# Optimization experiments

Measured on AMD Instinct MI355X. Metric: run time of the kernel, lower is better.

Reference implementation:

```python
import jax, jax.numpy as jnp
import numpy as np
from jax import lax

K = 3
STRIDE = 1
PAD = 1


def setup_inputs() -> dict:
    key = jax.random.key(0)
    k1, k2, k3, k4 = jax.random.split(key, 4)
    B, C, H, W = 4, 64, 128, 128
    O = 64
    x = jax.random.normal(k1, (B, C, H, W), dtype=jnp.float32)
    weight = jax.random.normal(k2, (O, C, K, K), dtype=jnp.float32) * 0.05
    bias = jax.random.normal(k3, (O,), dtype=jnp.float32) * 0.05
    # original zero-inits offset_conv (degenerate); use small random weights instead
    offset_w = jax.random.normal(k4, (2 * K * K, C, 3, 3), dtype=jnp.float32) * 0.01
    offset_b = jnp.zeros((2 * K * K,), dtype=jnp.float32)
    return {"x": x, "weight": weight, "bias": bias, "offset_w": offset_w, "offset_b": offset_b}


def _deform_conv(x, weight, bias, offset_w, offset_b):
    B, C, H, W = x.shape
    O = weight.shape[0]
    K2 = K * K
    # offset predictor: 3x3 conv, pad 1, stride 1 -> [B, 2*K2, H, W]
    offsets = lax.conv_general_dilated(
        x, offset_w, window_strides=(1, 1), padding=[(1, 1), (1, 1)],
        dimension_numbers=("NCHW", "OIHW", "NCHW")) + offset_b[None, :, None, None]

    Ho = (H - K + 2 * PAD) // STRIDE + 1
    Wo = (W - K + 2 * PAD) // STRIDE + 1
    padded = jnp.pad(x, ((0, 0), (0, 0), (PAD, PAD), (PAD, PAD)))
    Hp, Wp = H + 2 * PAD, W + 2 * PAD

    off_h = offsets[:, :K2, :Ho, :Wo]   # [B,K2,Ho,Wo]
    off_w = offsets[:, K2:, :Ho, :Wo]

    # kernel tap grid, flattened row-major: idx = kh*K + kw
    grid_h = jnp.repeat(jnp.arange(K, dtype=x.dtype), K)   # [K2]
    grid_w = jnp.tile(jnp.arange(K, dtype=x.dtype), K)
    center_h = (jnp.arange(Ho, dtype=x.dtype) * STRIDE)
    center_w = (jnp.arange(Wo, dtype=x.dtype) * STRIDE)

    # sampling positions in padded coords, per original: grid + offset + center + PAD
    pos_h = grid_h[None, :, None, None] + off_h + center_h[None, None, :, None] + PAD
    pos_w = grid_w[None, :, None, None] + off_w + center_w[None, None, None, :] + PAD
    pos_h = jnp.clip(pos_h, 0.0, Hp - 1)
    pos_w = jnp.clip(pos_w, 0.0, Wp - 1)

    h0 = jnp.floor(pos_h).astype(jnp.int32)
    w0 = jnp.floor(pos_w).astype(jnp.int32)
    h1 = jnp.clip(h0 + 1, 0, Hp - 1)
    w1 = jnp.clip(w0 + 1, 0, Wp - 1)

    wh0 = h1.astype(x.dtype) - pos_h
    ww0 = w1.astype(x.dtype) - pos_w
    wh1 = pos_h - h0.astype(x.dtype)
    ww1 = pos_w - w0.astype(x.dtype)

    def gather(p, hi, wi):  # p:[C,Hp,Wp], hi/wi:[K2,Ho,Wo] -> [C,K2,Ho,Wo]
        return p[:, hi, wi]

    g = jax.vmap(gather)
    v00 = g(padded, h0, w0)
    v01 = g(padded, h0, w1)
    v10 = g(padded, h1, w0)
    v11 = g(padded, h1, w1)

    e = lambda a: a[:, None]  # [B,K2,Ho,Wo] -> [B,1,K2,Ho,Wo]
    val = (v00 * e(wh0 * ww0) + v01 * e(wh0 * ww1)
           + v10 * e(wh1 * ww0) + v11 * e(wh1 * ww1))  # [B,C,K2,Ho,Wo]

    out = jnp.einsum("bckhw,ock->bohw", val, weight.reshape(O, C, K2))
    return out + bias[None, :, None, None]


def reference(x, weight, bias, offset_w, offset_b):
    return _deform_conv(x, weight, bias, offset_w, offset_b)
```

## Files before the change

kernel.cpp:

```cpp
#include <hip/hip_runtime.h>

#define BB 4
#define CC 64
#define OO 64
#define HH 128
#define WW 128
#define HP 131
#define WP 132
#define HW (HH*WW)

#define TH 8
#define TW 8
#define WR 15
#define WC 15
#define NWIN (WR*WC)
#define PXS 36

typedef __attribute__((ext_vector_type(8))) short short8;
typedef __attribute__((ext_vector_type(4))) float f32x4;

__device__ __forceinline__ unsigned f2b(float f) {
  unsigned u = __float_as_uint(f);
  return (u + 0x7fffu + ((u >> 16) & 1u)) >> 16;
}
__device__ __forceinline__ float blo(unsigned r) { return __uint_as_float(r << 16); }
__device__ __forceinline__ float bhi(unsigned r) { return __uint_as_float(r & 0xffff0000u); }
__device__ __forceinline__ unsigned pk2(float a, float b) { return f2b(a) | (f2b(b) << 16); }

__device__ __forceinline__ short8 lerp8(uint4 q00, uint4 q01, uint4 q10, uint4 q11,
                                        float ww0, float ww1, float wh0, float wh1) {
  unsigned c00[4] = {q00.x, q00.y, q00.z, q00.w};
  unsigned c01[4] = {q01.x, q01.y, q01.z, q01.w};
  unsigned c10[4] = {q10.x, q10.y, q10.z, q10.w};
  unsigned c11[4] = {q11.x, q11.y, q11.z, q11.w};
  union { unsigned u[4]; short8 v; } A;
#pragma unroll
  for (int t = 0; t < 4; ++t) {
    float tL = fmaf(blo(c01[t]), ww1, blo(c00[t]) * ww0);
    float bL = fmaf(blo(c11[t]), ww1, blo(c10[t]) * ww0);
    float tH = fmaf(bhi(c01[t]), ww1, bhi(c00[t]) * ww0);
    float bH = fmaf(bhi(c11[t]), ww1, bhi(c10[t]) * ww0);
    A.u[t] = pk2(fmaf(bL, wh1, tL * wh0), fmaf(bH, wh1, tH * wh0));
  }
  return A.v;
}

__global__ __launch_bounds__(256) void pad_kernel(const float* __restrict__ x,
                                                  unsigned* __restrict__ xp) {
  int i = blockIdx.x * 256 + threadIdx.x;
  if (i >= BB * HP * WP * 8) return;
  int c8 = i & 7;
  int t = i >> 3;
  int wp = t % WP;
  int t2 = t / WP;
  int hp = t2 % HP;
  int b = t2 / HP;
  uint4 v = make_uint4(0, 0, 0, 0);
  if (hp >= 1 && hp <= HH && wp >= 1 && wp <= WW) {
    const float* s = x + (((size_t)(b * CC + c8 * 8)) * HH + (hp - 1)) * WW + (wp - 1);
    v.x = pk2(s[0], s[HW]);
    v.y = pk2(s[2 * HW], s[3 * HW]);
    v.z = pk2(s[4 * HW], s[5 * HW]);
    v.w = pk2(s[6 * HW], s[7 * HW]);
  }
  *(uint4*)(xp + (size_t)t * 32 + c8 * 4) = v;
}

__global__ __launch_bounds__(256) void repackw_kernel(const float* __restrict__ wt,
                                                      const float* __restrict__ ow,
                                                      ushort* __restrict__ wbf,
                                                      ushort* __restrict__ owbf) {
  int i = blockIdx.x * 256 + threadIdx.x;
  if (i < 72 * 512) {
    int j = i & 7, lane = (i >> 3) & 63, T = i >> 9;
    int nt = T & 3, sh = (T >> 2) & 1, kk = T >> 3;
    int o = nt * 16 + (lane & 15);
    int c = sh * 32 + (lane >> 4) * 8 + j;
    wbf[i] = (ushort)f2b(wt[(o * CC + c) * 9 + kk]);
  } else if (i < 72 * 512 + 36 * 512) {
    int i2 = i - 72 * 512;
    int j = i2 & 7, lane = (i2 >> 3) & 63, T = i2 >> 9;
    int nt = T & 1, sh = (T >> 1) & 1, kk = T >> 2;
    int oc = nt * 16 + (lane & 15);
    int c = sh * 32 + (lane >> 4) * 8 + j;
    owbf[i2] = (oc < 18) ? (ushort)f2b(ow[(oc * CC + c) * 9 + kk]) : (ushort)0;
  }
}

__global__ __launch_bounds__(256, 3) void fused_deform(const unsigned* __restrict__ xp,
                                                       const ushort* __restrict__ wbf,
                                                       const ushort* __restrict__ owbf,
                                                       const float* __restrict__ obias,
                                                       const float* __restrict__ bias,
                                                       float* __restrict__ out) {
  __shared__ __align__(16) unsigned win[NWIN * PXS];
  __shared__ __align__(16) float obuf[64 * 20];

  int tid = threadIdx.x;
  int blk0 = blockIdx.x;
  int xcd = blk0 & 7, i = blk0 >> 3;
  int s = xcd * 8 + (i >> 4);
  int b = s >> 4, ht = s & 15, wtile = i & 15;
  int H0 = ht * TH, W0 = wtile * TW;
  int rlo = H0 - 1, clo = W0 - 1;

  int wave = tid >> 6, lane = tid & 63, lm = lane & 15, lq = lane >> 4;
  const unsigned* xpb = xp + (size_t)b * (HP * WP * 32);

  for (int q = tid; q < NWIN * 8; q += 256) {
    int px = q >> 3, ch = q & 7;
    int r = px / WC, c = px % WC;
    int pr = rlo + r, pc = clo + c;
    uint4 v = make_uint4(0, 0, 0, 0);
    if (pr >= 0 && pr <= HP - 1 && pc >= 0 && pc <= WP - 2)
      v = *(const uint4*)(xpb + ((size_t)pr * WP + pc) * 32 + ch * 4);
    *(uint4*)&win[px * PXS + ch * 4] = v;
  }
  __syncthreads();

  int row = 2 * wave + (lm >> 3);
  int col = lm & 7;
  int h = H0 + row, w = W0 + col;

  {
    short8 Ao0[9], Ao1[9];
#pragma unroll
    for (int kk = 0; kk < 9; ++kk) {
      int kh = kk / 3, kw = kk % 3;
      int widx = (row + kh + 1) * WC + (col + kw + 1);
      const unsigned* wp0 = &win[widx * PXS + lq * 4];
      Ao0[kk] = *(const short8*)wp0;
      Ao1[kk] = *(const short8*)(wp0 + 16);
    }
    f32x4 oacc[2];
    oacc[0] = (f32x4)0.0f; oacc[1] = (f32x4)0.0f;
#pragma unroll
    for (int nt = 0; nt < 2; ++nt) {
#pragma unroll
      for (int kk = 0; kk < 9; ++kk) {
        short8 b0 = *(const short8*)&owbf[(size_t)(kk * 4 + nt) * 512 + lane * 8];
        short8 b1 = *(const short8*)&owbf[(size_t)(kk * 4 + 2 + nt) * 512 + lane * 8];
        oacc[nt] = __builtin_amdgcn_mfma_f32_16x16x32_bf16(Ao0[kk], b0, oacc[nt], 0, 0, 0);
        oacc[nt] = __builtin_amdgcn_mfma_f32_16x16x32_bf16(Ao1[kk], b1, oacc[nt], 0, 0, 0);
      }
    }
#pragma unroll
    for (int nt = 0; nt < 2; ++nt) {
      int oc = nt * 16 + lm;
      if (oc < 18) {
        float bv = obias[oc];
        int idx = (oc < 9) ? (oc * 2) : ((oc - 9) * 2 + 1);
#pragma unroll
        for (int r2 = 0; r2 < 4; ++r2)
          obuf[(wave * 16 + lq * 4 + r2) * 20 + idx] = oacc[nt][r2] + bv;
      }
    }
  }
  __syncthreads();

  float orow[20];
  {
    const float* orp = &obuf[(wave * 16 + lm) * 20];
#pragma unroll
    for (int q = 0; q < 5; ++q) *(float4*)&orow[q * 4] = *(const float4*)(orp + q * 4);
  }

  f32x4 acc[4];
#pragma unroll
  for (int nt = 0; nt < 4; ++nt) acc[nt] = (f32x4)0.0f;

  bool okall = true;
#pragma unroll
  for (int kk = 0; kk < 9; ++kk) {
    int kh = kk / 3, kw = kk % 3;
    float ph = (((float)kh + orow[kk * 2]) + (float)h) + 1.0f;
    float pw = (((float)kw + orow[kk * 2 + 1]) + (float)w) + 1.0f;
    ph = fminf(fmaxf(ph, 0.0f), 129.0f);
    pw = fminf(fmaxf(pw, 0.0f), 129.0f);
    int h0 = (int)floorf(ph), w0 = (int)floorf(pw);
    int wr0 = h0 - rlo, wc0 = w0 - clo;
    okall &= (wr0 >= 0) & (wr0 <= WR - 2) & (wc0 >= 0) & (wc0 <= WC - 2);
  }

  if (__builtin_amdgcn_ballot_w64(okall) == ~0ull) {
    short8 Af0[9], Af1[9];
#pragma unroll
    for (int kk = 0; kk < 9; ++kk) {
      int kh = kk / 3, kw = kk % 3;
      float ph = (((float)kh + orow[kk * 2]) + (float)h) + 1.0f;
      float pw = (((float)kw + orow[kk * 2 + 1]) + (float)w) + 1.0f;
      ph = fminf(fmaxf(ph, 0.0f), 129.0f);
      pw = fminf(fmaxf(pw, 0.0f), 129.0f);
      float fh0 = floorf(ph), fw0 = floorf(pw);
      int h0 = (int)fh0, w0 = (int)fw0;
      float wh1 = ph - fh0, ww1 = pw - fw0;
      float wh0 = 1.0f - wh1, ww0 = 1.0f - ww1;
      const unsigned* pA = &win[((h0 - rlo) * WC + (w0 - clo)) * PXS + lq * 4];
      uint4 q00a = *(const uint4*)pA;
      uint4 q01a = *(const uint4*)(pA + PXS);
      uint4 q10a = *(const uint4*)(pA + WC * PXS);
      uint4 q11a = *(const uint4*)(pA + WC * PXS + PXS);
      uint4 q00b = *(const uint4*)(pA + 16);
      uint4 q01b = *(const uint4*)(pA + PXS + 16);
      uint4 q10b = *(const uint4*)(pA + WC * PXS + 16);
      uint4 q11b = *(const uint4*)(pA + WC * PXS + PXS + 16);
      Af0[kk] = lerp8(q00a, q01a, q10a, q11a, ww0, ww1, wh0, wh1);
      Af1[kk] = lerp8(q00b, q01b, q10b, q11b, ww0, ww1, wh0, wh1);
    }
#pragma unroll
    for (int nt = 0; nt < 4; ++nt) {
#pragma unroll
      for (int kk = 0; kk < 9; ++kk) {
        short8 b0 = *(const short8*)&wbf[(size_t)(kk * 8 + nt) * 512 + lane * 8];
        short8 b1 = *(const short8*)&wbf[(size_t)(kk * 8 + 4 + nt) * 512 + lane * 8];
        acc[nt] = __builtin_amdgcn_mfma_f32_16x16x32_bf16(Af0[kk], b0, acc[nt], 0, 0, 0);
        acc[nt] = __builtin_amdgcn_mfma_f32_16x16x32_bf16(Af1[kk], b1, acc[nt], 0, 0, 0);
      }
    }
  } else {
#pragma unroll 1
    for (int kk = 0; kk < 9; ++kk) {
      int kh = kk / 3, kw = kk % 3;
      float ph = (((float)kh + orow[kk * 2]) + (float)h) + 1.0f;
      float pw = (((float)kw + orow[kk * 2 + 1]) + (float)w) + 1.0f;
      ph = fminf(fmaxf(ph, 0.0f), 129.0f);
      pw = fminf(fmaxf(pw, 0.0f), 129.0f);
      float fh0 = floorf(ph), fw0 = floorf(pw);
      int h0 = (int)fh0, w0 = (int)fw0;
      float wh1 = ph - fh0, ww1 = pw - fw0;
      float wh0 = 1.0f - wh1, ww0 = 1.0f - ww1;
      const unsigned* pG = xpb + ((size_t)h0 * WP + w0) * 32 + lq * 4;
      uint4 q00a = *(const uint4*)pG;
      uint4 q01a = *(const uint4*)(pG + 32);
      uint4 q10a = *(const uint4*)(pG + WP * 32);
      uint4 q11a = *(const uint4*)(pG + WP * 32 + 32);
      uint4 q00b = *(const uint4*)(pG + 16);
      uint4 q01b = *(const uint4*)(pG + 48);
      uint4 q10b = *(const uint4*)(pG + WP * 32 + 16);
      uint4 q11b = *(const uint4*)(pG + WP * 32 + 48);
      short8 A0v = lerp8(q00a, q01a, q10a, q11a, ww0, ww1, wh0, wh1);
      short8 A1v = lerp8(q00b, q01b, q10b, q11b, ww0, ww1, wh0, wh1);
#pragma unroll
      for (int nt = 0; nt < 4; ++nt) {
        short8 b0 = *(const short8*)&wbf[(size_t)(kk * 8 + nt) * 512 + lane * 8];
        short8 b1 = *(const short8*)&wbf[(size_t)(kk * 8 + 4 + nt) * 512 + lane * 8];
        acc[nt] = __builtin_amdgcn_mfma_f32_16x16x32_bf16(A0v, b0, acc[nt], 0, 0, 0);
        acc[nt] = __builtin_amdgcn_mfma_f32_16x16x32_bf16(A1v, b1, acc[nt], 0, 0, 0);
      }
    }
  }

  {
    int px0 = lq * 4;
    int hrow = H0 + 2 * wave + (px0 >> 3);
    int wcol = W0 + (px0 & 7);
#pragma unroll
    for (int nt = 0; nt < 4; ++nt) {
      int o = nt * 16 + lm;
      float bv = bias[o];
      float4 st = make_float4(acc[nt][0] + bv, acc[nt][1] + bv, acc[nt][2] + bv, acc[nt][3] + bv);
      *(float4*)(out + ((size_t)(b * OO + o) * HH + hrow) * WW + wcol) = st;
    }
  }
}

extern "C" void kernel_launch(void* const* d_in, const int* in_sizes, int n_in,
                              void* d_out, int out_size, void* d_ws, size_t ws_size,
                              hipStream_t stream) {
  const float* x        = (const float*)d_in[0];
  const float* weight   = (const float*)d_in[1];
  const float* bias     = (const float*)d_in[2];
  const float* offset_w = (const float*)d_in[3];
  const float* offset_b = (const float*)d_in[4];
  float* out = (float*)d_out;

  unsigned* xp  = (unsigned*)d_ws;
  ushort* wbf  = (ushort*)(xp + (size_t)BB * HP * WP * 32);
  ushort* owbf = wbf + (size_t)72 * 512;

  pad_kernel<<<(BB * HP * WP * 8 + 255) / 256, 256, 0, stream>>>(x, xp);
  repackw_kernel<<<(72 * 512 + 36 * 512 + 255) / 256, 256, 0, stream>>>(weight, offset_w, wbf, owbf);
  fused_deform<<<1024, 256, 0, stream>>>(xp, wbf, owbf, offset_b, bias, out);
}
```

Baseline: 119.8 us.

## Restructure fused deform conv loops to cut registers and use hardware bf16 packing

Several changes land together. Manual bf16 rounding is replaced with the v_cvt_pk_bf16_f32 instruction, and the launch bound rises from 3 to 4 blocks per CU. The MFMA loops are reordered to be kk-outer, so per-tap A fragments are no longer all held live and register pressure drops. The window load is batched into registers before the LDS stores to expose memory-level parallelism, and the sampling positions are computed once and reused. The higher occupancy target could force spills, and the hardware convert may round differently in edge cases.

```diff
diff --git a/kernel.cpp b/kernel.cpp
--- a/kernel.cpp
+++ b/kernel.cpp
@@ -23,9 +23,13 @@
   unsigned u = __float_as_uint(f);
   return (u + 0x7fffu + ((u >> 16) & 1u)) >> 16;
 }
+__device__ __forceinline__ unsigned cvtpk(float lo, float hi) {
+  unsigned r;
+  asm("v_cvt_pk_bf16_f32 %0, %1, %2" : "=v"(r) : "v"(lo), "v"(hi));
+  return r;
+}
 __device__ __forceinline__ float blo(unsigned r) { return __uint_as_float(r << 16); }
 __device__ __forceinline__ float bhi(unsigned r) { return __uint_as_float(r & 0xffff0000u); }
-__device__ __forceinline__ unsigned pk2(float a, float b) { return f2b(a) | (f2b(b) << 16); }
 
 __device__ __forceinline__ short8 lerp8(uint4 q00, uint4 q01, uint4 q10, uint4 q11,
                                         float ww0, float ww1, float wh0, float wh1) {
@@ -40,7 +44,7 @@
     float bL = fmaf(blo(c11[t]), ww1, blo(c10[t]) * ww0);
     float tH = fmaf(bhi(c01[t]), ww1, bhi(c00[t]) * ww0);
     float bH = fmaf(bhi(c11[t]), ww1, bhi(c10[t]) * ww0);
-    A.u[t] = pk2(fmaf(bL, wh1, tL * wh0), fmaf(bH, wh1, tH * wh0));
+    A.u[t] = cvtpk(fmaf(bL, wh1, tL * wh0), fmaf(bH, wh1, tH * wh0));
   }
   return A.v;
 }
@@ -58,10 +62,10 @@
   uint4 v = make_uint4(0, 0, 0, 0);
   if (hp >= 1 && hp <= HH && wp >= 1 && wp <= WW) {
     const float* s = x + (((size_t)(b * CC + c8 * 8)) * HH + (hp - 1)) * WW + (wp - 1);
-    v.x = pk2(s[0], s[HW]);
-    v.y = pk2(s[2 * HW], s[3 * HW]);
-    v.z = pk2(s[4 * HW], s[5 * HW]);
-    v.w = pk2(s[6 * HW], s[7 * HW]);
+    v.x = cvtpk(s[0], s[HW]);
+    v.y = cvtpk(s[2 * HW], s[3 * HW]);
+    v.z = cvtpk(s[4 * HW], s[5 * HW]);
+    v.w = cvtpk(s[6 * HW], s[7 * HW]);
   }
   *(uint4*)(xp + (size_t)t * 32 + c8 * 4) = v;
 }
@@ -87,7 +91,7 @@
   }
 }
 
-__global__ __launch_bounds__(256, 3) void fused_deform(const unsigned* __restrict__ xp,
+__global__ __launch_bounds__(256, 4) void fused_deform(const unsigned* __restrict__ xp,
                                                        const ushort* __restrict__ wbf,
                                                        const ushort* __restrict__ owbf,
                                                        const float* __restrict__ obias,
@@ -107,14 +111,29 @@
   int wave = tid >> 6, lane = tid & 63, lm = lane & 15, lq = lane >> 4;
   const unsigned* xpb = xp + (size_t)b * (HP * WP * 32);
 
-  for (int q = tid; q < NWIN * 8; q += 256) {
-    int px = q >> 3, ch = q & 7;
-    int r = px / WC, c = px % WC;
-    int pr = rlo + r, pc = clo + c;
-    uint4 v = make_uint4(0, 0, 0, 0);
-    if (pr >= 0 && pr <= HP - 1 && pc >= 0 && pc <= WP - 2)
-      v = *(const uint4*)(xpb + ((size_t)pr * WP + pc) * 32 + ch * 4);
-    *(uint4*)&win[px * PXS + ch * 4] = v;
+  {
+    uint4 sv[8];
+#pragma unroll
+    for (int it = 0; it < 8; ++it) {
+      int q = tid + it * 256;
+      uint4 v = make_uint4(0, 0, 0, 0);
+      if (q < NWIN * 8) {
+        int px = q >> 3;
+        int r = px / WC, c = px % WC;
+        int pr = rlo + r, pc = clo + c;
+        if (pr >= 0 && pr <= HP - 1 && pc >= 0 && pc <= WP - 2)
+          v = *(const uint4*)(xpb + ((size_t)pr * WP + pc) * 32 + (q & 7) * 4);
+      }
+      sv[it] = v;
+    }
+#pragma unroll
+    for (int it = 0; it < 8; ++it) {
+      int q = tid + it * 256;
+      if (q < NWIN * 8) {
+        int px = q >> 3, ch = q & 7;
+        *(uint4*)&win[px * PXS + ch * 4] = sv[it];
+      }
+    }
   }
   __syncthreads();
 
@@ -123,77 +142,82 @@
   int h = H0 + row, w = W0 + col;
 
   {
-    short8 Ao0[9], Ao1[9];
+    f32x4 oacc0 = (f32x4)0.0f, oacc1 = (f32x4)0.0f;
 #pragma unroll
     for (int kk = 0; kk < 9; ++kk) {
+      const ushort* obp = owbf + (size_t)(kk * 4) * 512 + lane * 8;
+      short8 ob00 = *(const short8*)(obp);
+      short8 ob01 = *(const short8*)(obp + 512);
+      short8 ob10 = *(const short8*)(obp + 1024);
+      short8 ob11 = *(const short8*)(obp + 1536);
       int kh = kk / 3, kw = kk % 3;
       int widx = (row + kh + 1) * WC + (col + kw + 1);
       const unsigned* wp0 = &win[widx * PXS + lq * 4];
-      Ao0[kk] = *(const short8*)wp0;
-      Ao1[kk] = *(const short8*)(wp0 + 16);
-    }
-    f32x4 oacc[2];
-    oacc[0] = (f32x4)0.0f; oacc[1] = (f32x4)0.0f;
+      short8 Ao0 = *(const short8*)wp0;
+      short8 Ao1 = *(const short8*)(wp0 + 16);
+      oacc0 = __builtin_amdgcn_mfma_f32_16x16x32_bf16(Ao0, ob00, oacc0, 0, 0, 0);
+      oacc1 = __builtin_amdgcn_mfma_f32_16x16x32_bf16(Ao0, ob01, oacc1, 0, 0, 0);
+      oacc0 = __builtin_amdgcn_mfma_f32_16x16x32_bf16(Ao1, ob10, oacc0, 0, 0, 0);
+      oacc1 = __builtin_amdgcn_mfma_f32_16x16x32_bf16(Ao1, ob11, oacc1, 0, 0, 0);
+    }
 #pragma unroll
     for (int nt = 0; nt < 2; ++nt) {
-#pragma unroll
-      for (int kk = 0; kk < 9; ++kk) {
-        short8 b0 = *(const short8*)&owbf[(size_t)(kk * 4 + nt) * 512 + lane * 8];
-        short8 b1 = *(const short8*)&owbf[(size_t)(kk * 4 + 2 + nt) * 512 + lane * 8];
-        oacc[nt] = __builtin_amdgcn_mfma_f32_16x16x32_bf16(Ao0[kk], b0, oacc[nt], 0, 0, 0);
-        oacc[nt] = __builtin_amdgcn_mfma_f32_16x16x32_bf16(Ao1[kk], b1, oacc[nt], 0, 0, 0);
-      }
-    }
-#pragma unroll
-    for (int nt = 0; nt < 2; ++nt) {
+      f32x4 oa = nt ? oacc1 : oacc0;
       int oc = nt * 16 + lm;
       if (oc < 18) {
         float bv = obias[oc];
         int idx = (oc < 9) ? (oc * 2) : ((oc - 9) * 2 + 1);
 #pragma unroll
         for (int r2 = 0; r2 < 4; ++r2)
-          obuf[(wave * 16 + lq * 4 + r2) * 20 + idx] = oacc[nt][r2] + bv;
+          obuf[(wave * 16 + lq * 4 + r2) * 20 + idx] = oa[r2] + bv;
       }
     }
   }
   __syncthreads();
 
-  float orow[20];
+  float ph[9], pw[9];
+  bool okall = true;
   {
+    float orow[20];
     const float* orp = &obuf[(wave * 16 + lm) * 20];
 #pragma unroll
     for (int q = 0; q < 5; ++q) *(float4*)&orow[q * 4] = *(const float4*)(orp + q * 4);
-  }
-
-  f32x4 acc[4];
-#pragma unroll
-  for (int nt = 0; nt < 4; ++nt) acc[nt] = (f32x4)0.0f;
-
-  bool okall = true;
-#pragma unroll
-  for (int kk = 0; kk < 9; ++kk) {
-    int kh = kk / 3, kw = kk % 3;
-    float ph = (((float)kh + orow[kk * 2]) + (float)h) + 1.0f;
-    float pw = (((float)kw + orow[kk * 2 + 1]) + (float)w) + 1.0f;
-    ph = fminf(fmaxf(ph, 0.0f), 129.0f);
-    pw = fminf(fmaxf(pw, 0.0f), 129.0f);
-    int h0 = (int)floorf(ph), w0 = (int)floorf(pw);
-    int wr0 = h0 - rlo, wc0 = w0 - clo;
-    okall &= (wr0 >= 0) & (wr0 <= WR - 2) & (wc0 >= 0) & (wc0 <= WC - 2);
-  }
-
-  if (__builtin_amdgcn_ballot_w64(okall) == ~0ull) {
-    short8 Af0[9], Af1[9];
 #pragma unroll
     for (int kk = 0; kk < 9; ++kk) {
       int kh = kk / 3, kw = kk % 3;
-      float ph = (((float)kh + orow[kk * 2]) + (float)h) + 1.0f;
-      float pw = (((float)kw + orow[kk * 2 + 1]) + (float)w) + 1.0f;
-      ph = fminf(fmaxf(ph, 0.0f), 129.0f);
-      pw = fminf(fmaxf(pw, 0.0f), 129.0f);
-      float fh0 = floorf(ph), fw0 = floorf(pw);
+      float p_h = (((float)kh + orow[kk * 2]) + (float)h) + 1.0f;
+      float p_w = (((float)kw + orow[kk * 2 + 1]) + (float)w) + 1.0f;
+      p_h = fminf(fmaxf(p_h, 0.0f), 129.0f);
+      p_w = fminf(fmaxf(p_w, 0.0f), 129.0f);
+      ph[kk] = p_h;
+      pw[kk] = p_w;
+      int h0 = (int)floorf(p_h), w0 = (int)floorf(p_w);
+      int wr0 = h0 - rlo, wc0 = w0 - clo;
+      okall &= (wr0 >= 0) & (wr0 <= WR - 2) & (wc0 >= 0) & (wc0 <= WC - 2);
+    }
+  }
+
+  f32x4 acc[4];
+#pragma unroll
+  for (int nt = 0; nt < 4; ++nt) acc[nt] = (f32x4)0.0f;
+
+  if (__builtin_amdgcn_ballot_w64(okall) == ~0ull) {
+#pragma unroll
+    for (int kk = 0; kk < 9; ++kk) {
+      const ushort* bp = wbf + (size_t)kk * 4096 + lane * 8;
+      short8 b00 = *(const short8*)(bp);
+      short8 b01 = *(const short8*)(bp + 512);
+      short8 b02 = *(const short8*)(bp + 1024);
+      short8 b03 = *(const short8*)(bp + 1536);
+      short8 b10 = *(const short8*)(bp + 2048);
+      short8 b11 = *(const short8*)(bp + 2560);
+      short8 b12 = *(const short8*)(bp + 3072);
+      short8 b13 = *(const short8*)(bp + 3584);
+
+      float p_h = ph[kk], p_w = pw[kk];
+      float fh0 = floorf(p_h), fw0 = floorf(p_w);
       int h0 = (int)fh0, w0 = (int)fw0;
-      float wh1 = ph - fh0, ww1 = pw - fw0;
+      float wh1 = p_h - fh0, ww1 = p_w - fw0;
       float wh0 = 1.0f - wh1, ww0 = 1.0f - ww1;
       const unsigned* pA = &win[((h0 - rlo) * WC + (w0 - clo)) * PXS + lq * 4];
       uint4 q00a = *(const uint4*)pA;
@@ -204,30 +228,25 @@
       uint4 q01b = *(const uint4*)(pA + PXS + 16);
       uint4 q10b = *(const uint4*)(pA + WC * PXS + 16);
       uint4 q11b = *(const uint4*)(pA + WC * PXS + PXS + 16);
-      Af0[kk] = lerp8(q00a, q01a, q10a, q11a, ww0, ww1, wh0, wh1);
-      Af1[kk] = lerp8(q00b, q01b, q10b, q11b, ww0, ww1, wh0, wh1);
-    }
-#pragma unroll
-    for (int nt = 0; nt < 4; ++nt) {
-#pragma unroll
-      for (int kk = 0; kk < 9; ++kk) {
-        short8 b0 = *(const short8*)&wbf[(size_t)(kk * 8 + nt) * 512 + lane * 8];
-        short8 b1 = *(const short8*)&wbf[(size_t)(kk * 8 + 4 + nt) * 512 + lane * 8];
-        acc[nt] = __builtin_amdgcn_mfma_f32_16x16x32_bf16(Af0[kk], b0, acc[nt], 0, 0, 0);
-        acc[nt] = __builtin_amdgcn_mfma_f32_16x16x32_bf16(Af1[kk], b1, acc[nt], 0, 0, 0);
-      }
+      short8 Af0 = lerp8(q00a, q01a, q10a, q11a, ww0, ww1, wh0, wh1);
+      short8 Af1 = lerp8(q00b, q01b, q10b, q11b, ww0, ww1, wh0, wh1);
+
+      acc[0] = __builtin_amdgcn_mfma_f32_16x16x32_bf16(Af0, b00, acc[0], 0, 0, 0);
+      acc[1] = __builtin_amdgcn_mfma_f32_16x16x32_bf16(Af0, b01, acc[1], 0, 0, 0);
+      acc[2] = __builtin_amdgcn_mfma_f32_16x16x32_bf16(Af0, b02, acc[2], 0, 0, 0);
+      acc[3] = __builtin_amdgcn_mfma_f32_16x16x32_bf16(Af0, b03, acc[3], 0, 0, 0);
+      acc[0] = __builtin_amdgcn_mfma_f32_16x16x32_bf16(Af1, b10, acc[0], 0, 0, 0);
+      acc[1] = __builtin_amdgcn_mfma_f32_16x16x32_bf16(Af1, b11, acc[1], 0, 0, 0);
+      acc[2] = __builtin_amdgcn_mfma_f32_16x16x32_bf16(Af1, b12, acc[2], 0, 0, 0);
+      acc[3] = __builtin_amdgcn_mfma_f32_16x16x32_bf16(Af1, b13, acc[3], 0, 0, 0);
     }
   } else {
-#pragma unroll 1
+#pragma unroll
     for (int kk = 0; kk < 9; ++kk) {
-      int kh = kk / 3, kw = kk % 3;
-      float ph = (((float)kh + orow[kk * 2]) + (float)h) + 1.0f;
-      float pw = (((float)kw + orow[kk * 2 + 1]) + (float)w) + 1.0f;
-      ph = fminf(fmaxf(ph, 0.0f), 129.0f);
-      pw = fminf(fmaxf(pw, 0.0f), 129.0f);
-      float fh0 = floorf(ph), fw0 = floorf(pw);
+      float p_h = ph[kk], p_w = pw[kk];
+      float fh0 = floorf(p_h), fw0 = floorf(p_w);
       int h0 = (int)fh0, w0 = (int)fw0;
-      float wh1 = ph - fh0, ww1 = pw - fw0;
+      float wh1 = p_h - fh0, ww1 = p_w - fw0;
       float wh0 = 1.0f - wh1, ww0 = 1.0f - ww1;
       const unsigned* pG = xpb + ((size_t)h0 * WP + w0) * 32 + lq * 4;
       uint4 q00a = *(const uint4*)pG;
@@ -240,13 +259,15 @@
       uint4 q11b = *(const uint4*)(pG + WP * 32 + 48);
       short8 A0v = lerp8(q00a, q01a, q10a, q11a, ww0, ww1, wh0, wh1);
       short8 A1v = lerp8(q00b, q01b, q10b, q11b, ww0, ww1, wh0, wh1);
-#pragma unroll
-      for (int nt = 0; nt < 4; ++nt) {
-        short8 b0 = *(const short8*)&wbf[(size_t)(kk * 8 + nt) * 512 + lane * 8];
-        short8 b1 = *(const short8*)&wbf[(size_t)(kk * 8 + 4 + nt) * 512 + lane * 8];
-        acc[nt] = __builtin_amdgcn_mfma_f32_16x16x32_bf16(A0v, b0, acc[nt], 0, 0, 0);
-        acc[nt] = __builtin_amdgcn_mfma_f32_16x16x32_bf16(A1v, b1, acc[nt], 0, 0, 0);
-      }
+      const ushort* bp = wbf + (size_t)kk * 4096 + lane * 8;
+      acc[0] = __builtin_amdgcn_mfma_f32_16x16x32_bf16(A0v, *(const short8*)(bp), acc[0], 0, 0, 0);
+      acc[1] = __builtin_amdgcn_mfma_f32_16x16x32_bf16(A0v, *(const short8*)(bp + 512), acc[1], 0, 0, 0);
+      acc[2] = __builtin_amdgcn_mfma_f32_16x16x32_bf16(A0v, *(const short8*)(bp + 1024), acc[2], 0, 0, 0);
+      acc[3] = __builtin_amdgcn_mfma_f32_16x16x32_bf16(A0v, *(const short8*)(bp + 1536), acc[3], 0, 0, 0);
+      acc[0] = __builtin_amdgcn_mfma_f32_16x16x32_bf16(A1v, *(const short8*)(bp + 2048), acc[0], 0, 0, 0);
+      acc[1] = __builtin_amdgcn_mfma_f32_16x16x32_bf16(A1v, *(const short8*)(bp + 2560), acc[1], 0, 0, 0);
+      acc[2] = __builtin_amdgcn_mfma_f32_16x16x32_bf16(A1v, *(const short8*)(bp + 3072), acc[2], 0, 0, 0);
+      acc[3] = __builtin_amdgcn_mfma_f32_16x16x32_bf16(A1v, *(const short8*)(bp + 3584), acc[3], 0, 0, 0);
     }
   }
 
```

After: 105.9 us. 1.13x faster.
